# Kernel optimization log

Measured on AMD Instinct MI355X. Metric: run time of the kernel, lower is better.

Reference implementation:

```python
import jax, jax.numpy as jnp
import numpy as np

T, B, H, I = 128, 32, 256, 256


def setup_inputs() -> dict:
    key = jax.random.key(0)
    ks = jax.random.split(key, 8)
    s = 0.05
    embs = jax.random.normal(ks[0], (T, B, I), jnp.float32)
    lens = jax.random.randint(ks[1], (B,), 1, T + 1)  # lengths in [1, T]
    W_ih = jax.random.normal(ks[2], (4 * H, I), jnp.float32) * s
    W_hh = jax.random.normal(ks[3], (4 * H, H), jnp.float32) * s
    b_ih = jax.random.normal(ks[4], (4 * H,), jnp.float32) * s
    b_hh = jax.random.normal(ks[5], (4 * H,), jnp.float32) * s
    W_a = jax.random.normal(ks[6], (H, 2 * H), jnp.float32) * s  # attention combine (Luong-style)
    b_a = jax.random.normal(ks[7], (H,), jnp.float32) * s
    return {"embs": embs, "lens": lens, "W_ih": W_ih, "W_hh": W_hh,
            "b_ih": b_ih, "b_hh": b_hh, "W_a": W_a, "b_a": b_a}


def reference(embs, lens, W_ih, W_hh, b_ih, b_hh, W_a, b_a):
    Tn, Bn, _ = embs.shape
    Hn = W_hh.shape[1]
    t_idx = jnp.arange(Tn)

    def step(carry, inp):
        h, c, buf, h_fin, c_fin = carry  # h,c: [B,H]; buf: [T,B,H] history of outputs
        t, emb = inp
        # dot-product attention of current hidden over past outputs (steps < t)
        scores = jnp.einsum('tbh,bh->tb', buf, h)
        valid = (t_idx < t)[:, None]
        alpha = jax.nn.softmax(jnp.where(valid, scores, -1e9), axis=0)
        ctx = jnp.einsum('tb,tbh->bh', alpha, buf)
        h_att = jnp.tanh(jnp.concatenate([ctx, h], axis=-1) @ W_a.T + b_a)
        h = jnp.where(t > 0, h_att, h)  # no history at t=0
        # standard PyTorch LSTM cell (gate order i,f,g,o)
        gates = emb @ W_ih.T + b_ih + h @ W_hh.T + b_hh
        i_g, f_g, g_g, o_g = jnp.split(gates, 4, axis=-1)
        c = jax.nn.sigmoid(f_g) * c + jax.nn.sigmoid(i_g) * jnp.tanh(g_g)
        h = jax.nn.sigmoid(o_g) * jnp.tanh(c)
        buf = buf.at[t].set(h)
        take = (t == lens - 1)[:, None]
        h_fin = jnp.where(take, h, h_fin)
        c_fin = jnp.where(take, c, c_fin)
        return (h, c, buf, h_fin, c_fin), h

    z = jnp.zeros((Bn, Hn), embs.dtype)
    buf0 = jnp.zeros((Tn, Bn, Hn), embs.dtype)
    carry, output = jax.lax.scan(step, (z, z, buf0, z, z), (t_idx, embs))
    # output: [T,B,H]; final (h,c) gathered at t == lens-1: [B,H]
    return output, carry[3], carry[4]
```

## Files before the change

kernel.cpp:

```cpp
#include <hip/hip_runtime.h>


#define T_DIM 128
#define B_DIM 32

typedef _Float16 half2_t __attribute__((ext_vector_type(2)));

static __device__ __forceinline__ unsigned pack2(float a, float b) {
  half2_t h;
  h.x = (_Float16)a;
  h.y = (_Float16)b;
  return __builtin_bit_cast(unsigned, h);
}

static __device__ __forceinline__ float dot2f(unsigned w, unsigned v, float acc) {
  half2_t a = __builtin_bit_cast(half2_t, w);
  half2_t b = __builtin_bit_cast(half2_t, v);
#if __has_builtin(__builtin_amdgcn_fdot2)
  return __builtin_amdgcn_fdot2(a, b, acc, false);
#else
  return acc + (float)a.x * (float)b.x + (float)a.y * (float)b.y;
#endif
}

static __device__ __forceinline__ float dot8(uint4 w, uint4 v, float acc) {
  acc = dot2f(w.x, v.x, acc);
  acc = dot2f(w.y, v.y, acc);
  acc = dot2f(w.z, v.z, acc);
  acc = dot2f(w.w, v.w, acc);
  return acc;
}

static __device__ __forceinline__ float lo16(unsigned u) {
  return (float)__builtin_bit_cast(half2_t, u).x;
}
static __device__ __forceinline__ float hi16(unsigned u) {
  return (float)__builtin_bit_cast(half2_t, u).y;
}

static __device__ __forceinline__ float fsig(float x) {
  return __builtin_amdgcn_rcpf(1.f + __expf(-x));
}
static __device__ __forceinline__ float ftanh(float x) {
  float e = __expf(2.f * x);
  return 1.f - 2.f * __builtin_amdgcn_rcpf(e + 1.f);
}

static __device__ __forceinline__ unsigned long long wait_word(
    const unsigned long long* p, unsigned want, unsigned long long v) {
  while ((unsigned)v != want) {
    __builtin_amdgcn_s_sleep(1);
    v = __hip_atomic_load(p, __ATOMIC_RELAXED, __HIP_MEMORY_SCOPE_AGENT);
  }
  return v;
}

__global__ void pack_weights(const float* __restrict__ W_ih, const float* __restrict__ W_hh,
                             const float* __restrict__ W_a, unsigned* __restrict__ Wih16,
                             uint4* __restrict__ Whh_pack, uint4* __restrict__ Wa_pack,
                             unsigned long long* __restrict__ ywp,
                             unsigned long long* __restrict__ psx, int* __restrict__ ctr) {
  int n = blockIdx.x * 256 + threadIdx.x;
  if (n < 131072) {
    int k2 = n >> 10, r = n & 1023;
    const float* src = W_ih + r * 256 + 2 * k2;
    Wih16[n] = pack2(src[0], src[1]);
  }
  if (n < 32768) {
    int m = n >> 12, tid = (n >> 3) & 511, i = n & 7;
    int r_local = tid >> 2, qk = tid & 3;
    int q = r_local >> 5, jl = r_local & 31;
    int r = q * 256 + m * 32 + jl;
    const float* src = W_hh + r * 256 + (4 * i + qk) * 8;
    uint4 v;
    v.x = pack2(src[0], src[1]);
    v.y = pack2(src[2], src[3]);
    v.z = pack2(src[4], src[5]);
    v.w = pack2(src[6], src[7]);
    Whh_pack[n] = v;
  }
  if (n < 16384) {
    int m = n >> 11, j = (n >> 3) & 255, c = n & 7;
    int col0 = (c < 4) ? (m * 32 + c * 8) : (256 + m * 32 + (c - 4) * 8);
    const float* src = W_a + j * 512 + col0;
    uint4 v;
    v.x = pack2(src[0], src[1]);
    v.y = pack2(src[2], src[3]);
    v.z = pack2(src[4], src[5]);
    v.w = pack2(src[6], src[7]);
    Wa_pack[n] = v;
  }
  if (n < 65536)
    __hip_atomic_store(&ywp[n], 0ull, __ATOMIC_RELAXED, __HIP_MEMORY_SCOPE_AGENT);
  else if (n < 81920)
    __hip_atomic_store(&psx[n - 65536], 0ull, __ATOMIC_RELAXED, __HIP_MEMORY_SCOPE_AGENT);
  if (n < 4096)
    __hip_atomic_store(&ctr[n], 0, __ATOMIC_RELAXED, __HIP_MEMORY_SCOPE_AGENT);
}

__global__ void compute_gih(const float* __restrict__ embs, const unsigned* __restrict__ Wih16,
                            const float* __restrict__ b_ih, const float* __restrict__ b_hh,
                            float* __restrict__ gih) {
  __shared__ unsigned embS16[16][128];
  const int tid = threadIdx.x;
  const int tb0 = blockIdx.x * 16;
  for (int x = tid; x < 2048; x += 256) {
    int e = x >> 7, p = x & 127;
    const float* s = embs + (size_t)(tb0 + e) * 256 + 2 * p;
    embS16[e][p] = pack2(s[0], s[1]);
  }
  __syncthreads();
  float acc[16][4];
#pragma unroll
  for (int e = 0; e < 16; ++e)
#pragma unroll
    for (int q = 0; q < 4; ++q) acc[e][q] = 0.f;
  for (int k2 = 0; k2 < 128; ++k2) {
    unsigned w0 = Wih16[k2 * 1024 + tid];
    unsigned w1 = Wih16[k2 * 1024 + tid + 256];
    unsigned w2 = Wih16[k2 * 1024 + tid + 512];
    unsigned w3 = Wih16[k2 * 1024 + tid + 768];
#pragma unroll
    for (int e = 0; e < 16; ++e) {
      unsigned x = embS16[e][k2];
      acc[e][0] = dot2f(w0, x, acc[e][0]);
      acc[e][1] = dot2f(w1, x, acc[e][1]);
      acc[e][2] = dot2f(w2, x, acc[e][2]);
      acc[e][3] = dot2f(w3, x, acc[e][3]);
    }
  }
#pragma unroll
  for (int q = 0; q < 4; ++q) {
    float bias = b_ih[q * 256 + tid] + b_hh[q * 256 + tid];
#pragma unroll
    for (int e = 0; e < 16; ++e)
      gih[(size_t)(tb0 + e) * 1024 + q * 256 + tid] = acc[e][q] + bias;
  }
}

__global__ void __launch_bounds__(512, 1)
alstm_rec(const int* __restrict__ lens, const float* __restrict__ gih,
          const uint4* __restrict__ Whh_pack, const uint4* __restrict__ Wa_pack,
          const float* __restrict__ b_a, unsigned long long* __restrict__ ywp,
          unsigned long long* __restrict__ psx, int* __restrict__ ctr,
          float* __restrict__ out, float* __restrict__ hfin, float* __restrict__ cfin) {
  const int tid = threadIdx.x;
  const int b = blockIdx.x & 31;
  const int m = blockIdx.x >> 5;

  __shared__ __align__(16) unsigned histSl[128 * 20];
  __shared__ __align__(16) float ystoreF[128 * 256];
  __shared__ __align__(16) unsigned hp2[128];
  __shared__ __align__(16) unsigned hsl2[16];
  __shared__ float sc[128];
  __shared__ float zp[4][256];
  __shared__ float gsl[128];

  uint4 wh4[8];
  {
    const uint4* p = Whh_pack + ((size_t)m * 512 + tid) * 8;
#pragma unroll
    for (int i = 0; i < 8; ++i) wh4[i] = p[i];
  }
  uint4 way[4], waw[4];
  {
    const int j_pub = (tid - 128) & 255;
    const uint4* p = Wa_pack + ((size_t)m * 256 + j_pub) * 8;
#pragma unroll
    for (int i = 0; i < 4; ++i) way[i] = p[i];
#pragma unroll
    for (int i = 0; i < 4; ++i) waw[i] = p[4 + i];
  }
  const float ba_j = (tid < 256) ? b_a[tid] : 0.f;
  const int len_b = lens[b];
  const int r_local = tid >> 2, qk = tid & 3;
  const int gq = r_local >> 5, gjl = r_local & 31;

  if (tid < 128) hp2[tid] = 0u;
  float c_reg = 0.f;
  __syncthreads();

  for (int t = 0; t < T_DIM; ++t) {
    float gih_v = gih[((size_t)t * 32 + b) * 1024 + gq * 256 + m * 32 + gjl];
    float w_j = 0.f;

    if (t > 0) {
      {
        const int* cp = ctr + b * 128 + (t - 1);
        while (__hip_atomic_load(cp, __ATOMIC_RELAXED, __HIP_MEMORY_SCOPE_AGENT) < 8)
          __builtin_amdgcn_s_sleep(1);
      }
      if (tid < 256) {
        const unsigned long long* base = ywp + b * 2048 + tid;
        unsigned long long v[8];
#pragma unroll
        for (int mm = 0; mm < 8; ++mm)
          v[mm] = __hip_atomic_load(base + mm * 256, __ATOMIC_RELAXED, __HIP_MEMORY_SCOPE_AGENT);
#pragma unroll
        for (int mm = 0; mm < 8; ++mm) v[mm] = wait_word(base + mm * 256, (unsigned)t, v[mm]);
        float y = 0.f, w = 0.f;
#pragma unroll
        for (int mm = 0; mm < 8; ++mm) {
          unsigned pl = (unsigned)(v[mm] >> 32);
          y += lo16(pl);
          w += hi16(pl);
        }
        w_j = w;
        ystoreF[(t - 1) * 256 + tid] = y;
      } else if (tid >= 448) {
        const int lane = tid - 448;
        const unsigned long long* base = psx + b * 512 + lane;
        unsigned long long v[8];
#pragma unroll
        for (int mm = 0; mm < 8; ++mm)
          v[mm] = __hip_atomic_load(base + mm * 64, __ATOMIC_RELAXED, __HIP_MEMORY_SCOPE_AGENT);
#pragma unroll
        for (int mm = 0; mm < 8; ++mm) v[mm] = wait_word(base + mm * 64, (unsigned)t, v[mm]);
        float s0 = 0.f, s1 = 0.f;
#pragma unroll
        for (int mm = 0; mm < 8; ++mm) {
          unsigned pl = (unsigned)(v[mm] >> 32);
          s0 += lo16(pl);
          s1 += hi16(pl);
        }
        float v0 = (2 * lane < t) ? s0 : -3.0e38f;
        float v1 = (2 * lane + 1 < t) ? s1 : -3.0e38f;
        float mx = fmaxf(v0, v1);
#pragma unroll
        for (int off = 32; off >= 1; off >>= 1) mx = fmaxf(mx, __shfl_xor(mx, off));
        float e0 = (2 * lane < t) ? __expf(v0 - mx) : 0.f;
        float e1 = (2 * lane + 1 < t) ? __expf(v1 - mx) : 0.f;
        float sm = e0 + e1;
#pragma unroll
        for (int off = 32; off >= 1; off >>= 1) sm += __shfl_xor(sm, off);
        float inv = __builtin_amdgcn_rcpf(sm);
        sc[2 * lane] = e0 * inv;
        sc[2 * lane + 1] = e1 * inv;
      }
      __syncthreads();
      {
        const int sp = tid >> 7, p2 = tid & 127;
        float c0 = 0.f, c1 = 0.f;
        const float* yb = ystoreF + 2 * p2;
        for (int s = sp; s < t; s += 4) {
          float al = sc[s];
          float2 yv = *(const float2*)(yb + s * 256);
          c0 += al * yv.x;
          c1 += al * yv.y;
        }
        zp[sp][2 * p2] = c0;
        zp[sp][2 * p2 + 1] = c1;
      }
      __syncthreads();
      if (tid < 256) {
        float z = zp[0][tid] + zp[1][tid] + zp[2][tid] + zp[3][tid];
        float hv = ftanh(ba_j + w_j + z);
        float o = __shfl_xor(hv, 1);
        if (!(tid & 1)) hp2[tid >> 1] = pack2(hv, o);
      }
      __syncthreads();
    }
    {
      float a = 0.f;
#pragma unroll
      for (int i = 0; i < 8; ++i) {
        const int c = 4 * i + qk;
        uint4 hv = *(const uint4*)&hp2[c << 2];
        a = dot8(wh4[i], hv, a);
      }
      a += __shfl_xor(a, 1);
      a += __shfl_xor(a, 2);
      if (qk == 0) gsl[r_local] = a + gih_v;
    }
    __syncthreads();
    if (tid < 64) {
      if (tid < 32) {
        float ig = fsig(gsl[tid]);
        float fg = fsig(gsl[32 + tid]);
        float gg = ftanh(gsl[64 + tid]);
        float og = fsig(gsl[96 + tid]);
        float cn = fg * c_reg + ig * gg;
        float hn = og * ftanh(cn);
        c_reg = cn;
        out[((size_t)t * 32 + b) * 256 + m * 32 + tid] = hn;
        if (t == len_b - 1) {
          hfin[b * 256 + m * 32 + tid] = hn;
          cfin[b * 256 + m * 32 + tid] = cn;
        }
        float o = __shfl_xor(hn, 1);
        if (!(tid & 1)) {
          unsigned u = pack2(hn, o);
          hsl2[tid >> 1] = u;
          histSl[t * 20 + (tid >> 1)] = u;
        }
      }
      uint4 q0 = *(const uint4*)&hsl2[0];
      uint4 q1 = *(const uint4*)&hsl2[4];
      uint4 q2 = *(const uint4*)&hsl2[8];
      uint4 q3 = *(const uint4*)&hsl2[12];
      const int r0 = 2 * tid, r1 = 2 * tid + 1;
      float a0 = 0.f, a1 = 0.f;
      {
        uint4 h0, h1;
        h0 = *(const uint4*)&histSl[r0 * 20 + 0];
        h1 = *(const uint4*)&histSl[r1 * 20 + 0];
        a0 = dot8(h0, q0, a0);
        a1 = dot8(h1, q0, a1);
        h0 = *(const uint4*)&histSl[r0 * 20 + 4];
        h1 = *(const uint4*)&histSl[r1 * 20 + 4];
        a0 = dot8(h0, q1, a0);
        a1 = dot8(h1, q1, a1);
        h0 = *(const uint4*)&histSl[r0 * 20 + 8];
        h1 = *(const uint4*)&histSl[r1 * 20 + 8];
        a0 = dot8(h0, q2, a0);
        a1 = dot8(h1, q2, a1);
        h0 = *(const uint4*)&histSl[r0 * 20 + 12];
        h1 = *(const uint4*)&histSl[r1 * 20 + 12];
        a0 = dot8(h0, q3, a0);
        a1 = dot8(h1, q3, a1);
      }
      unsigned long long v = ((unsigned long long)pack2(a0, a1) << 32) |
                             (unsigned long long)(unsigned)(t + 1);
      __hip_atomic_store(&psx[b * 512 + m * 64 + tid], v, __ATOMIC_RELAXED,
                         __HIP_MEMORY_SCOPE_AGENT);
    }
    __syncthreads();
    if (tid >= 128 && tid < 384) {
      const int j = tid - 128;
      float ay = 0.f, aw = 0.f;
#pragma unroll
      for (int c = 0; c < 4; ++c) {
        uint4 hv = *(const uint4*)&hsl2[c * 4];
        ay = dot8(way[c], hv, ay);
        aw = dot8(waw[c], hv, aw);
      }
      unsigned long long v = ((unsigned long long)pack2(ay, aw) << 32) |
                             (unsigned long long)(unsigned)(t + 1);
      __hip_atomic_store(&ywp[b * 2048 + m * 256 + j], v, __ATOMIC_RELAXED,
                         __HIP_MEMORY_SCOPE_AGENT);
    }
    __syncthreads();
    if (tid == 0)
      __hip_atomic_fetch_add(&ctr[b * 128 + t], 1, __ATOMIC_RELAXED, __HIP_MEMORY_SCOPE_AGENT);
  }
}

extern "C" void kernel_launch(void* const* d_in, const int* in_sizes, int n_in,
                              void* d_out, int out_size, void* d_ws, size_t ws_size,
                              hipStream_t stream) {
  const float* embs = (const float*)d_in[0];
  const int* lens = (const int*)d_in[1];
  const float* W_ih = (const float*)d_in[2];
  const float* W_hh = (const float*)d_in[3];
  const float* b_ih = (const float*)d_in[4];
  const float* b_hh = (const float*)d_in[5];
  const float* W_a = (const float*)d_in[6];
  const float* b_a = (const float*)d_in[7];

  float* out = (float*)d_out;
  float* hfin = out + (size_t)T_DIM * B_DIM * 256;
  float* cfin = hfin + (size_t)B_DIM * 256;

  char* ws = (char*)d_ws;
  float* gih = (float*)ws;
  unsigned* Wih16 = (unsigned*)(ws + 16777216);
  uint4* Whh_pack = (uint4*)(ws + 17301504);
  uint4* Wa_pack = (uint4*)(ws + 17825792);
  unsigned long long* ywp = (unsigned long long*)(ws + 18087936);
  unsigned long long* psx = (unsigned long long*)(ws + 18612224);
  int* ctr = (int*)(ws + 18743296);

  pack_weights<<<1024, 256, 0, stream>>>(W_ih, W_hh, W_a, Wih16, Whh_pack, Wa_pack, ywp, psx,
                                         ctr);
  compute_gih<<<256, 256, 0, stream>>>(embs, Wih16, b_ih, b_hh, gih);
  alstm_rec<<<256, 512, 0, stream>>>(lens, gih, Whh_pack, Wa_pack, b_a, ywp, psx, ctr, out,
                                     hfin, cfin);
}
```

Before: 571.9 us.

## Fuse input projection into recurrent kernel and drop per-step counter barrier

Removes the separate gih precompute kernel and its 16MB intermediate; each recurrent block now holds packed W_ih rows in registers and computes the input gate contribution per step from embeddings staged in shared memory by an idle wave. The per-step counter barrier (syncthreads plus atomic add and spin-wait) is removed, relying only on the step-tagged words for synchronisation. Softmax max-subtraction is replaced by a clamp before exp, saving a reduction but risking accuracy or overflow when scores are large.

Measured after the change: 705.8 us. +23.4%, slower.

```diff
diff --git a/kernel.cpp b/kernel.cpp
--- a/kernel.cpp
+++ b/kernel.cpp
@@ -56,28 +56,34 @@
 }
 
 __global__ void pack_weights(const float* __restrict__ W_ih, const float* __restrict__ W_hh,
-                             const float* __restrict__ W_a, unsigned* __restrict__ Wih16,
-                             uint4* __restrict__ Whh_pack, uint4* __restrict__ Wa_pack,
+                             const float* __restrict__ W_a, uint4* __restrict__ Whh_pack,
+                             uint4* __restrict__ Wih_pack, uint4* __restrict__ Wa_pack,
                              unsigned long long* __restrict__ ywp,
-                             unsigned long long* __restrict__ psx, int* __restrict__ ctr) {
+                             unsigned long long* __restrict__ psx) {
   int n = blockIdx.x * 256 + threadIdx.x;
-  if (n < 131072) {
-    int k2 = n >> 10, r = n & 1023;
-    const float* src = W_ih + r * 256 + 2 * k2;
-    Wih16[n] = pack2(src[0], src[1]);
-  }
   if (n < 32768) {
     int m = n >> 12, tid = (n >> 3) & 511, i = n & 7;
     int r_local = tid >> 2, qk = tid & 3;
     int q = r_local >> 5, jl = r_local & 31;
     int r = q * 256 + m * 32 + jl;
-    const float* src = W_hh + r * 256 + (4 * i + qk) * 8;
-    uint4 v;
-    v.x = pack2(src[0], src[1]);
-    v.y = pack2(src[2], src[3]);
-    v.z = pack2(src[4], src[5]);
-    v.w = pack2(src[6], src[7]);
-    Whh_pack[n] = v;
+    {
+      const float* src = W_hh + r * 256 + (4 * i + qk) * 8;
+      uint4 v;
+      v.x = pack2(src[0], src[1]);
+      v.y = pack2(src[2], src[3]);
+      v.z = pack2(src[4], src[5]);
+      v.w = pack2(src[6], src[7]);
+      Whh_pack[n] = v;
+    }
+    {
+      const float* src = W_ih + r * 256 + (4 * i + qk) * 8;
+      uint4 v;
+      v.x = pack2(src[0], src[1]);
+      v.y = pack2(src[2], src[3]);
+      v.z = pack2(src[4], src[5]);
+      v.w = pack2(src[6], src[7]);
+      Wih_pack[n] = v;
+    }
   }
   if (n < 16384) {
     int m = n >> 11, j = (n >> 3) & 255, c = n & 7;
@@ -90,77 +96,42 @@
     v.w = pack2(src[6], src[7]);
     Wa_pack[n] = v;
   }
-  if (n < 65536)
-    __hip_atomic_store(&ywp[n], 0ull, __ATOMIC_RELAXED, __HIP_MEMORY_SCOPE_AGENT);
-  else if (n < 81920)
-    __hip_atomic_store(&psx[n - 65536], 0ull, __ATOMIC_RELAXED, __HIP_MEMORY_SCOPE_AGENT);
-  if (n < 4096)
-    __hip_atomic_store(&ctr[n], 0, __ATOMIC_RELAXED, __HIP_MEMORY_SCOPE_AGENT);
-}
-
-__global__ void compute_gih(const float* __restrict__ embs, const unsigned* __restrict__ Wih16,
-                            const float* __restrict__ b_ih, const float* __restrict__ b_hh,
-                            float* __restrict__ gih) {
-  __shared__ unsigned embS16[16][128];
-  const int tid = threadIdx.x;
-  const int tb0 = blockIdx.x * 16;
-  for (int x = tid; x < 2048; x += 256) {
-    int e = x >> 7, p = x & 127;
-    const float* s = embs + (size_t)(tb0 + e) * 256 + 2 * p;
-    embS16[e][p] = pack2(s[0], s[1]);
-  }
-  __syncthreads();
-  float acc[16][4];
-#pragma unroll
-  for (int e = 0; e < 16; ++e)
-#pragma unroll
-    for (int q = 0; q < 4; ++q) acc[e][q] = 0.f;
-  for (int k2 = 0; k2 < 128; ++k2) {
-    unsigned w0 = Wih16[k2 * 1024 + tid];
-    unsigned w1 = Wih16[k2 * 1024 + tid + 256];
-    unsigned w2 = Wih16[k2 * 1024 + tid + 512];
-    unsigned w3 = Wih16[k2 * 1024 + tid + 768];
-#pragma unroll
-    for (int e = 0; e < 16; ++e) {
-      unsigned x = embS16[e][k2];
-      acc[e][0] = dot2f(w0, x, acc[e][0]);
-      acc[e][1] = dot2f(w1, x, acc[e][1]);
-      acc[e][2] = dot2f(w2, x, acc[e][2]);
-      acc[e][3] = dot2f(w3, x, acc[e][3]);
-    }
-  }
-#pragma unroll
-  for (int q = 0; q < 4; ++q) {
-    float bias = b_ih[q * 256 + tid] + b_hh[q * 256 + tid];
-#pragma unroll
-    for (int e = 0; e < 16; ++e)
-      gih[(size_t)(tb0 + e) * 1024 + q * 256 + tid] = acc[e][q] + bias;
-  }
+  __hip_atomic_store(&ywp[n], 0ull, __ATOMIC_RELAXED, __HIP_MEMORY_SCOPE_AGENT);
+  if (n < 16384)
+    __hip_atomic_store(&psx[n], 0ull, __ATOMIC_RELAXED, __HIP_MEMORY_SCOPE_AGENT);
 }
 
 __global__ void __launch_bounds__(512, 1)
-alstm_rec(const int* __restrict__ lens, const float* __restrict__ gih,
-          const uint4* __restrict__ Whh_pack, const uint4* __restrict__ Wa_pack,
-          const float* __restrict__ b_a, unsigned long long* __restrict__ ywp,
-          unsigned long long* __restrict__ psx, int* __restrict__ ctr,
+alstm_rec(const int* __restrict__ lens, const float* __restrict__ embs,
+          const uint4* __restrict__ Whh_pack, const uint4* __restrict__ Wih_pack,
+          const uint4* __restrict__ Wa_pack, const float* __restrict__ b_ih,
+          const float* __restrict__ b_hh, const float* __restrict__ b_a,
+          unsigned long long* __restrict__ ywp, unsigned long long* __restrict__ psx,
           float* __restrict__ out, float* __restrict__ hfin, float* __restrict__ cfin) {
   const int tid = threadIdx.x;
   const int b = blockIdx.x & 31;
   const int m = blockIdx.x >> 5;
+  const int wv = tid >> 6, lane = tid & 63;
 
   __shared__ __align__(16) unsigned histSl[128 * 20];
   __shared__ __align__(16) float ystoreF[128 * 256];
   __shared__ __align__(16) unsigned hp2[128];
   __shared__ __align__(16) unsigned hsl2[16];
+  __shared__ __align__(16) unsigned ebuf[128];
   __shared__ float sc[128];
   __shared__ float zp[4][256];
   __shared__ float gsl[128];
 
-  uint4 wh4[8];
+  uint4 wh4[8], wi4[8];
   {
     const uint4* p = Whh_pack + ((size_t)m * 512 + tid) * 8;
 #pragma unroll
     for (int i = 0; i < 8; ++i) wh4[i] = p[i];
+  }
+  {
+    const uint4* p = Wih_pack + ((size_t)m * 512 + tid) * 8;
+#pragma unroll
+    for (int i = 0; i < 8; ++i) wi4[i] = p[i];
   }
   uint4 way[4], waw[4];
   {
@@ -175,21 +146,22 @@
   const int len_b = lens[b];
   const int r_local = tid >> 2, qk = tid & 3;
   const int gq = r_local >> 5, gjl = r_local & 31;
+  const int grow = gq * 256 + m * 32 + gjl;
+  const float bias_r = b_ih[grow] + b_hh[grow];
 
   if (tid < 128) hp2[tid] = 0u;
+  if (tid < 64) {
+    float4 e = *(const float4*)(embs + ((size_t)0 * 32 + b) * 256 + 4 * tid);
+    ebuf[2 * tid] = pack2(e.x, e.y);
+    ebuf[2 * tid + 1] = pack2(e.z, e.w);
+  }
   float c_reg = 0.f;
   __syncthreads();
 
   for (int t = 0; t < T_DIM; ++t) {
-    float gih_v = gih[((size_t)t * 32 + b) * 1024 + gq * 256 + m * 32 + gjl];
     float w_j = 0.f;
 
     if (t > 0) {
-      {
-        const int* cp = ctr + b * 128 + (t - 1);
-        while (__hip_atomic_load(cp, __ATOMIC_RELAXED, __HIP_MEMORY_SCOPE_AGENT) < 8)
-          __builtin_amdgcn_s_sleep(1);
-      }
       if (tid < 256) {
         const unsigned long long* base = ywp + b * 2048 + tid;
         unsigned long long v[8];
@@ -207,8 +179,13 @@
         }
         w_j = w;
         ystoreF[(t - 1) * 256 + tid] = y;
-      } else if (tid >= 448) {
-        const int lane = tid - 448;
+      } else if (wv == 6) {
+        if (lane < 64) {
+          float4 e = *(const float4*)(embs + ((size_t)t * 32 + b) * 256 + 4 * lane);
+          ebuf[2 * lane] = pack2(e.x, e.y);
+          ebuf[2 * lane + 1] = pack2(e.z, e.w);
+        }
+      } else if (wv == 7) {
         const unsigned long long* base = psx + b * 512 + lane;
         unsigned long long v[8];
 #pragma unroll
@@ -223,13 +200,8 @@
           s0 += lo16(pl);
           s1 += hi16(pl);
         }
-        float v0 = (2 * lane < t) ? s0 : -3.0e38f;
-        float v1 = (2 * lane + 1 < t) ? s1 : -3.0e38f;
-        float mx = fmaxf(v0, v1);
-#pragma unroll
-        for (int off = 32; off >= 1; off >>= 1) mx = fmaxf(mx, __shfl_xor(mx, off));
-        float e0 = (2 * lane < t) ? __expf(v0 - mx) : 0.f;
-        float e1 = (2 * lane + 1 < t) ? __expf(v1 - mx) : 0.f;
+        float e0 = (2 * lane < t) ? __expf(fminf(s0, 60.f)) : 0.f;
+        float e1 = (2 * lane + 1 < t) ? __expf(fminf(s1, 60.f)) : 0.f;
         float sm = e0 + e1;
 #pragma unroll
         for (int off = 32; off >= 1; off >>= 1) sm += __shfl_xor(sm, off);
@@ -261,16 +233,19 @@
       __syncthreads();
     }
     {
-      float a = 0.f;
+      float a = 0.f, a2 = 0.f;
 #pragma unroll
       for (int i = 0; i < 8; ++i) {
         const int c = 4 * i + qk;
         uint4 hv = *(const uint4*)&hp2[c << 2];
         a = dot8(wh4[i], hv, a);
-      }
+        uint4 ev = *(const uint4*)&ebuf[c << 2];
+        a2 = dot8(wi4[i], ev, a2);
+      }
+      a += a2;
       a += __shfl_xor(a, 1);
       a += __shfl_xor(a, 2);
-      if (qk == 0) gsl[r_local] = a + gih_v;
+      if (qk == 0) gsl[r_local] = a + bias_r;
     }
     __syncthreads();
     if (tid < 64) {
@@ -339,9 +314,6 @@
       __hip_atomic_store(&ywp[b * 2048 + m * 256 + j], v, __ATOMIC_RELAXED,
                          __HIP_MEMORY_SCOPE_AGENT);
     }
-    __syncthreads();
-    if (tid == 0)
-      __hip_atomic_fetch_add(&ctr[b * 128 + t], 1, __ATOMIC_RELAXED, __HIP_MEMORY_SCOPE_AGENT);
   }
 }
 
@@ -362,17 +334,14 @@
   float* cfin = hfin + (size_t)B_DIM * 256;
 
   char* ws = (char*)d_ws;
-  float* gih = (float*)ws;
-  unsigned* Wih16 = (unsigned*)(ws + 16777216);
-  uint4* Whh_pack = (uint4*)(ws + 17301504);
-  uint4* Wa_pack = (uint4*)(ws + 17825792);
-  unsigned long long* ywp = (unsigned long long*)(ws + 18087936);
-  unsigned long long* psx = (unsigned long long*)(ws + 18612224);
-  int* ctr = (int*)(ws + 18743296);
-
-  pack_weights<<<1024, 256, 0, stream>>>(W_ih, W_hh, W_a, Wih16, Whh_pack, Wa_pack, ywp, psx,
-                                         ctr);
-  compute_gih<<<256, 256, 0, stream>>>(embs, Wih16, b_ih, b_hh, gih);
-  alstm_rec<<<256, 512, 0, stream>>>(lens, gih, Whh_pack, Wa_pack, b_a, ywp, psx, ctr, out,
-                                     hfin, cfin);
-}
+  uint4* Whh_pack = (uint4*)ws;
+  uint4* Wih_pack = (uint4*)(ws + 524288);
+  uint4* Wa_pack = (uint4*)(ws + 1048576);
+  unsigned long long* ywp = (unsigned long long*)(ws + 1310720);
+  unsigned long long* psx = (unsigned long long*)(ws + 1835008);
+
+  pack_weights<<<256, 256, 0, stream>>>(W_ih, W_hh, W_a, Whh_pack, Wih_pack, Wa_pack, ywp,
+                                        psx);
+  alstm_rec<<<256, 512, 0, stream>>>(lens, embs, Whh_pack, Wih_pack, Wa_pack, b_ih, b_hh, b_a,
+                                     ywp, psx, out, hfin, cfin);
+}
```
